# Kernel optimization log

Measured on AMD Instinct MI355X. Metric: run time of the kernel, lower is better.

## Reference

```python
import jax, jax.numpy as jnp
import numpy as np

EPS = 1e-5  # BatchNorm eps


def cbr(x, W, g, b, m, v):
    # 1x1 Conv (no bias) + inference BatchNorm + ReLU
    # x: [B,Cin,H,W], W: [Cout,Cin]
    y = jnp.einsum('oc,bchw->bohw', W, x)
    inv = g / jnp.sqrt(v + EPS)            # [Cout]
    y = y * inv[None, :, None, None] + (b - m * inv)[None, :, None, None]
    return jax.nn.relu(y)


def setup_inputs() -> dict:
    key = jax.random.key(0)
    ks = jax.random.split(key, 32)
    B, C, R, H, W = 4, 2048, 512, 64, 64
    d = {"feature": jax.random.normal(ks[0], (B, C, H, W), jnp.float32)}
    idx = 1
    for name, (cin, cout) in [("r", (C, R)), ("q", (R, R)), ("k", (R, R)), ("v", (R, R)), ("u", (R, C))]:
        d[name + "_W"] = jax.random.normal(ks[idx], (cout, cin), jnp.float32) * 0.02
        d[name + "_g"] = jax.random.uniform(ks[idx + 1], (cout,), jnp.float32)
        d[name + "_b"] = jax.random.normal(ks[idx + 2], (cout,), jnp.float32) * 0.1
        d[name + "_m"] = jax.random.normal(ks[idx + 3], (cout,), jnp.float32) * 0.1
        d[name + "_v"] = jax.random.uniform(ks[idx + 4], (cout,), jnp.float32)
        idx += 5
    return d


def reference(feature, r_W, r_g, r_b, r_m, r_v,
              q_W, q_g, q_b, q_m, q_v,
              k_W, k_g, k_b, k_m, k_v,
              v_W, v_g, v_b, v_m, v_v,
              u_W, u_g, u_b, u_m, u_v):
    B, C, H, W = feature.shape
    f = cbr(feature, r_W, r_g, r_b, r_m, r_v)          # [B,R,H,W]
    R = f.shape[1]
    N = H * W
    q = cbr(f, q_W, q_g, q_b, q_m, q_v).reshape(B, R, N)
    k = cbr(f, k_W, k_g, k_b, k_m, k_v).reshape(B, R, N)
    v = cbr(f, v_W, v_g, v_b, v_m, v_v).reshape(B, R, N)
    # similarity map over all spatial positions: [B,N,N]
    attn = jax.nn.softmax(jnp.einsum('bcn,bcm->bnm', q, k), axis=-1)
    upd = jnp.einsum('bnm,bcm->bnc', attn, v)          # [B,N,R]
    upd = upd.reshape(B, H, W, R).transpose(0, 3, 1, 2)  # [B,R,H,W]
    return cbr(f + upd, u_W, u_g, u_b, u_m, u_v)       # [B,C,H,W]
```

## Files before the change

kernel.cpp:

```cpp
#include <hip/hip_runtime.h>

#define EPSV 1e-5f

typedef unsigned short u16;
typedef __attribute__((ext_vector_type(8))) _Float16 half8;
typedef __attribute__((ext_vector_type(4))) float floatx4;

__device__ __forceinline__ float h2f(u16 h) {
    return (float)__builtin_bit_cast(_Float16, h);
}
__device__ __forceinline__ u16 f2h(float f) {
    _Float16 h = (_Float16)f;
    return __builtin_bit_cast(u16, h);
}

template <int MODE, typename OUTT>
__global__ __launch_bounds__(256)
void gemm_nt(const u16* __restrict__ A, const u16* __restrict__ B,
             OUTT* __restrict__ C_,
             const float* __restrict__ inv_, const float* __restrict__ beta_,
             const u16* __restrict__ addf,
             int K, int ldA, int ldB, int ldC,
             long strideA, long strideB, long strideC)
{
    __shared__ u16 As[4][128 * 32];
    __shared__ u16 Bs[4][128 * 32];

    const int tid = threadIdx.x;
    const int w = tid >> 6;
    const int l = tid & 63;

    int bx = blockIdx.x, by = blockIdx.y, bz = blockIdx.z;
    {
        const int gx = gridDim.x, gy = gridDim.y;
        const int nwg = gx * gy * (int)gridDim.z;
        if ((nwg & 7) == 0) {
            const int lin = bx + gx * (by + gy * bz);
            const int swz = (lin & 7) * (nwg >> 3) + (lin >> 3);
            bx = swz % gx;
            const int t = swz / gx;
            by = t % gy;
            bz = t / gy;
        }
    }
    const int j0 = bx * 128;
    const int i0 = by * 128;

    const u16* Ab = A + (long)bz * strideA;
    const u16* Bb = B + (long)bz * strideB;

    const int srow = w * 16 + (l >> 2);
    const int skel = (l & 3) * 8;

    const int i_base = (w >> 1) * 64;
    const int j_base = (w & 1) * 64;
    const int lm = l & 15;
    const int kq = l >> 4;

    floatx4 acc[4][4];
    #pragma unroll
    for (int a = 0; a < 4; ++a)
        #pragma unroll
        for (int b = 0; b < 4; ++b) acc[a][b] = (floatx4)(0.0f);

    auto stage = [&](int buf, int k0) {
        const u16* ga0 = Ab + (long)(i0 + srow) * ldA + k0 + skel;
        const u16* ga1 = Ab + (long)(i0 + 64 + srow) * ldA + k0 + skel;
        const u16* gb0 = Bb + (long)(j0 + srow) * ldB + k0 + skel;
        const u16* gb1 = Bb + (long)(j0 + 64 + srow) * ldB + k0 + skel;
        char* la0 = (char*)&As[buf][0] + w * 1024;
        char* la1 = (char*)&As[buf][0] + 4096 + w * 1024;
        char* lb0 = (char*)&Bs[buf][0] + w * 1024;
        char* lb1 = (char*)&Bs[buf][0] + 4096 + w * 1024;
        __builtin_amdgcn_global_load_lds(
            (const __attribute__((address_space(1))) unsigned int*)(const void*)ga0,
            (__attribute__((address_space(3))) unsigned int*)(void*)la0, 16, 0, 0);
        __builtin_amdgcn_global_load_lds(
            (const __attribute__((address_space(1))) unsigned int*)(const void*)ga1,
            (__attribute__((address_space(3))) unsigned int*)(void*)la1, 16, 0, 0);
        __builtin_amdgcn_global_load_lds(
            (const __attribute__((address_space(1))) unsigned int*)(const void*)gb0,
            (__attribute__((address_space(3))) unsigned int*)(void*)lb0, 16, 0, 0);
        __builtin_amdgcn_global_load_lds(
            (const __attribute__((address_space(1))) unsigned int*)(const void*)gb1,
            (__attribute__((address_space(3))) unsigned int*)(void*)lb1, 16, 0, 0);
    };

    const int nt = K >> 5;
    stage(0, 0);
    if (nt > 1) stage(1, 32);

    for (int t = 0; t < nt; ++t) {
        if (t + 2 < nt) {
            stage((t + 2) & 3, (t + 2) << 5);
            asm volatile("s_waitcnt vmcnt(8)" ::: "memory");
        } else if (t + 1 < nt) {
            asm volatile("s_waitcnt vmcnt(4)" ::: "memory");
        } else {
            asm volatile("s_waitcnt vmcnt(0)" ::: "memory");
        }
        __builtin_amdgcn_s_barrier();
        __builtin_amdgcn_sched_barrier(0);

        const u16* Ac = &As[t & 3][0];
        const u16* Bc = &Bs[t & 3][0];
        half8 af[4], bf[4];
        #pragma unroll
        for (int tt = 0; tt < 4; ++tt) {
            af[tt] = *(const half8*)&Ac[(i_base + tt * 16 + lm) * 32 + kq * 8];
            bf[tt] = *(const half8*)&Bc[(j_base + tt * 16 + lm) * 32 + kq * 8];
        }
        #pragma unroll
        for (int ti = 0; ti < 4; ++ti)
            #pragma unroll
            for (int tj = 0; tj < 4; ++tj)
                acc[ti][tj] = __builtin_amdgcn_mfma_f32_16x16x32_f16(
                    af[ti], bf[tj], acc[ti][tj], 0, 0, 0);
    }

    OUTT* Cb = C_ + (long)bz * strideC;
    const u16* addb = (MODE == 3) ? addf + (long)bz * strideC : nullptr;
    #pragma unroll
    for (int ti = 0; ti < 4; ++ti) {
        #pragma unroll
        for (int tj = 0; tj < 4; ++tj) {
            const int jj = j0 + j_base + tj * 16 + lm;
            float cinv = 0.f, cbeta = 0.f;
            if (MODE == 1) { cinv = inv_[jj]; cbeta = beta_[jj]; }
            #pragma unroll
            for (int r = 0; r < 4; ++r) {
                const int ii = i0 + i_base + ti * 16 + kq * 4 + r;
                float val = acc[ti][tj][r];
                if (MODE == 1) val = fmaxf(val * cinv + cbeta, 0.0f);
                if (MODE == 2) {
                    float iv = inv_[ii], bt = beta_[ii];
                    val = fmaxf(val * iv + bt, 0.0f);
                }
                if (MODE == 3) val += h2f(addb[(long)ii * ldC + jj]);
                if (sizeof(OUTT) == 4) {
                    ((float*)Cb)[(long)ii * ldC + jj] = val;
                } else {
                    ((u16*)Cb)[(long)ii * ldC + jj] = f2h(val);
                }
            }
        }
    }
}

__global__ __launch_bounds__(256)
void conv_weight(const float* __restrict__ W, const float* __restrict__ g,
                 const float* __restrict__ b, const float* __restrict__ m,
                 const float* __restrict__ v,
                 u16* __restrict__ Wb, float* __restrict__ inv_,
                 float* __restrict__ beta_, int cout, long n)
{
    for (long idx = (long)blockIdx.x * 256 + threadIdx.x; idx < n;
         idx += (long)gridDim.x * 256)
        Wb[idx] = f2h(W[idx]);
    int c = blockIdx.x * 256 + threadIdx.x;
    if (c < cout) {
        float iv = g[c] * rsqrtf(v[c] + EPSV);
        inv_[c] = iv;
        beta_[c] = b[c] - m[c] * iv;
    }
}

__global__ __launch_bounds__(256)
void transpose_conv(const float* __restrict__ in, u16* __restrict__ out,
                    int C, int N)
{
    __shared__ float t[32][33];
    const int n0 = blockIdx.x * 32, c0 = blockIdx.y * 32;
    const float* inb = in + (long)blockIdx.z * C * N;
    u16* outb = out + (long)blockIdx.z * C * N;
    const int tx = threadIdx.x & 31, ty = threadIdx.x >> 5;
    #pragma unroll
    for (int rr = 0; rr < 32; rr += 8)
        t[ty + rr][tx] = inb[(long)(c0 + ty + rr) * N + n0 + tx];
    __syncthreads();
    #pragma unroll
    for (int rr = 0; rr < 32; rr += 8)
        outb[(long)(n0 + ty + rr) * C + c0 + tx] = f2h(t[tx][ty + rr]);
}

__global__ __launch_bounds__(256)
void softmax_f16(const float* __restrict__ S, u16* __restrict__ P)
{
    __shared__ float buf[4096];
    __shared__ float red[256];
    const float* p = S + (long)blockIdx.y * 4096 * 4096 + (long)blockIdx.x * 4096;
    u16* o = P + (long)blockIdx.y * 4096 * 4096 + (long)blockIdx.x * 4096;
    const int tid = threadIdx.x;

    float lmax = -3.4e38f;
    for (int i = tid; i < 4096; i += 256) {
        float x = p[i];
        buf[i] = x;
        lmax = fmaxf(lmax, x);
    }
    red[tid] = lmax;
    __syncthreads();
    for (int s = 128; s > 0; s >>= 1) {
        if (tid < s) red[tid] = fmaxf(red[tid], red[tid + s]);
        __syncthreads();
    }
    const float mx = red[0];
    __syncthreads();

    float lsum = 0.0f;
    for (int i = tid; i < 4096; i += 256) {
        float e = __expf(buf[i] - mx);
        buf[i] = e;
        lsum += e;
    }
    red[tid] = lsum;
    __syncthreads();
    for (int s = 128; s > 0; s >>= 1) {
        if (tid < s) red[tid] += red[tid + s];
        __syncthreads();
    }
    const float invs = 1.0f / red[0];
    __syncthreads();

    for (int i = tid; i < 4096; i += 256) o[i] = f2h(buf[i] * invs);
}

extern "C" void kernel_launch(void* const* d_in, const int* in_sizes, int n_in,
                              void* d_out, int out_size, void* d_ws, size_t ws_size,
                              hipStream_t stream)
{
    (void)in_sizes; (void)n_in; (void)out_size; (void)ws_size;
    constexpr int B = 4, C = 2048, R = 512, N = 4096;
    constexpr long NR = (long)N * R;
    constexpr long NC = (long)N * C;
    constexpr long NN = (long)N * N;
    constexpr long NQK = (long)N * 1024;

    const float* feature = (const float*)d_in[0];
    const float* W_[5]  = {(const float*)d_in[1],  (const float*)d_in[6],
                           (const float*)d_in[11], (const float*)d_in[16],
                           (const float*)d_in[21]};
    const float* G_[5]  = {(const float*)d_in[2],  (const float*)d_in[7],
                           (const float*)d_in[12], (const float*)d_in[17],
                           (const float*)d_in[22]};
    const float* Bb_[5] = {(const float*)d_in[3],  (const float*)d_in[8],
                           (const float*)d_in[13], (const float*)d_in[18],
                           (const float*)d_in[23]};
    const float* M_[5]  = {(const float*)d_in[4],  (const float*)d_in[9],
                           (const float*)d_in[14], (const float*)d_in[19],
                           (const float*)d_in[24]};
    const float* V_[5]  = {(const float*)d_in[5],  (const float*)d_in[10],
                           (const float*)d_in[15], (const float*)d_in[20],
                           (const float*)d_in[25]};

    char* base = (char*)d_ws;
    size_t off = 0;
    float* S     = (float*)base;
    u16*   featT = (u16*)base;
    off += (size_t)B * NN * 4;
    u16* fT  = (u16*)(base + off);                     off += (size_t)B * NR * 2;
    u16* qkT = (u16*)(base + off);                     off += (size_t)B * NQK * 2;
    u16* vC  = (u16*)(base + off);                     off += (size_t)B * NR * 2;
    u16* gT  = (u16*)(base + off);                     off += (size_t)B * NR * 2;
    u16* Pc  = (u16*)(base + off);                     off += (size_t)B * NN * 2;
    u16* Wb_r  = (u16*)(base + off);  off += (size_t)R * C * 2;
    u16* WbQK  = (u16*)(base + off);  off += (size_t)1024 * R * 2;
    u16* Wb_v  = (u16*)(base + off);  off += (size_t)R * R * 2;
    u16* Wb_u  = (u16*)(base + off);  off += (size_t)C * R * 2;
    off = (off + 255) & ~(size_t)255;
    float* inv_r  = (float*)(base + off);  off += 8192;
    float* beta_r = (float*)(base + off);  off += 8192;
    float* invQK  = (float*)(base + off);  off += 8192;
    float* betaQK = (float*)(base + off);  off += 8192;
    float* inv_v  = (float*)(base + off);  off += 8192;
    float* beta_v = (float*)(base + off);  off += 8192;
    float* inv_u  = (float*)(base + off);  off += 8192;
    float* beta_u = (float*)(base + off);  off += 8192;

    float* out = (float*)d_out;
    const dim3 blk(256);

    conv_weight<<<512, blk, 0, stream>>>(W_[0], G_[0], Bb_[0], M_[0], V_[0],
                                         Wb_r, inv_r, beta_r, R, (long)R * C);
    conv_weight<<<512, blk, 0, stream>>>(W_[1], G_[1], Bb_[1], M_[1], V_[1],
                                         WbQK, invQK, betaQK, R, (long)R * R);
    conv_weight<<<512, blk, 0, stream>>>(W_[2], G_[2], Bb_[2], M_[2], V_[2],
                                         WbQK + (size_t)R * R, invQK + R, betaQK + R,
                                         R, (long)R * R);
    conv_weight<<<512, blk, 0, stream>>>(W_[3], G_[3], Bb_[3], M_[3], V_[3],
                                         Wb_v, inv_v, beta_v, R, (long)R * R);
    conv_weight<<<512, blk, 0, stream>>>(W_[4], G_[4], Bb_[4], M_[4], V_[4],
                                         Wb_u, inv_u, beta_u, C, (long)C * R);

    transpose_conv<<<dim3(N / 32, C / 32, B), blk, 0, stream>>>(feature, featT, C, N);

    gemm_nt<1, u16><<<dim3(R / 128, N / 128, B), blk, 0, stream>>>(
        featT, Wb_r, fT, inv_r, beta_r, nullptr,
        C, C, C, R, NC, 0, NR);

    gemm_nt<1, u16><<<dim3(1024 / 128, N / 128, B), blk, 0, stream>>>(
        fT, WbQK, qkT, invQK, betaQK, nullptr,
        R, R, R, 1024, NR, 0, NQK);

    gemm_nt<2, u16><<<dim3(N / 128, R / 128, B), blk, 0, stream>>>(
        Wb_v, fT, vC, inv_v, beta_v, nullptr,
        R, R, R, N, 0, NR, NR);

    gemm_nt<0, float><<<dim3(N / 128, N / 128, B), blk, 0, stream>>>(
        qkT, qkT + 512, S, nullptr, nullptr, nullptr,
        R, 1024, 1024, N, NQK, NQK, NN);

    softmax_f16<<<dim3(N, B), blk, 0, stream>>>(S, Pc);

    gemm_nt<3, u16><<<dim3(R / 128, N / 128, B), blk, 0, stream>>>(
        Pc, vC, gT, nullptr, nullptr, fT,
        N, N, N, R, NN, NR, NR);

    gemm_nt<2, float><<<dim3(N / 128, C / 128, B), blk, 0, stream>>>(
        Wb_u, gT, out, inv_u, beta_u, nullptr,
        R, R, R, N, 0, NR, NC);
}
```

Measured before the change: 801.5 us.

## Add double-buffer GEMM variant and split QK+softmax per batch

```diff
diff --git a/kernel.cpp b/kernel.cpp
--- a/kernel.cpp
+++ b/kernel.cpp
@@ -14,7 +14,7 @@
     return __builtin_bit_cast(u16, h);
 }
 
-template <int MODE, typename OUTT>
+template <int MODE, typename OUTT, int DEEP>
 __global__ __launch_bounds__(256)
 void gemm_nt(const u16* __restrict__ A, const u16* __restrict__ B,
              OUTT* __restrict__ C_,
@@ -23,8 +23,9 @@
              int K, int ldA, int ldB, int ldC,
              long strideA, long strideB, long strideC)
 {
-    __shared__ u16 As[4][128 * 32];
-    __shared__ u16 Bs[4][128 * 32];
+    constexpr int NBUF = DEEP ? 4 : 2;
+    __shared__ u16 As[NBUF][128 * 32];
+    __shared__ u16 Bs[NBUF][128 * 32];
 
     const int tid = threadIdx.x;
     const int w = tid >> 6;
@@ -87,35 +88,61 @@
     };
 
     const int nt = K >> 5;
-    stage(0, 0);
-    if (nt > 1) stage(1, 32);
-
-    for (int t = 0; t < nt; ++t) {
-        if (t + 2 < nt) {
-            stage((t + 2) & 3, (t + 2) << 5);
-            asm volatile("s_waitcnt vmcnt(8)" ::: "memory");
-        } else if (t + 1 < nt) {
-            asm volatile("s_waitcnt vmcnt(4)" ::: "memory");
-        } else {
-            asm volatile("s_waitcnt vmcnt(0)" ::: "memory");
+
+    if (DEEP) {
+        stage(0, 0);
+        if (nt > 1) stage(1, 32);
+        for (int t = 0; t < nt; ++t) {
+            if (t + 2 < nt) {
+                stage((t + 2) & 3, (t + 2) << 5);
+                asm volatile("s_waitcnt vmcnt(8)" ::: "memory");
+            } else if (t + 1 < nt) {
+                asm volatile("s_waitcnt vmcnt(4)" ::: "memory");
+            } else {
+                asm volatile("s_waitcnt vmcnt(0)" ::: "memory");
+            }
+            __builtin_amdgcn_s_barrier();
+            __builtin_amdgcn_sched_barrier(0);
+
+            const u16* Ac = &As[t & 3][0];
+            const u16* Bc = &Bs[t & 3][0];
+            half8 af[4], bf[4];
+            #pragma unroll
+            for (int tt = 0; tt < 4; ++tt) {
+                af[tt] = *(const half8*)&Ac[(i_base + tt * 16 + lm) * 32 + kq * 8];
+                bf[tt] = *(const half8*)&Bc[(j_base + tt * 16 + lm) * 32 + kq * 8];
+            }
+            #pragma unroll
+            for (int ti = 0; ti < 4; ++ti)
+                #pragma unroll
+                for (int tj = 0; tj < 4; ++tj)
+                    acc[ti][tj] = __builtin_amdgcn_mfma_f32_16x16x32_f16(
+                        af[ti], bf[tj], acc[ti][tj], 0, 0, 0);
         }
-        __builtin_amdgcn_s_barrier();
-        __builtin_amdgcn_sched_barrier(0);
-
-        const u16* Ac = &As[t & 3][0];
-        const u16* Bc = &Bs[t & 3][0];
-        half8 af[4], bf[4];
-        #pragma unroll
-        for (int tt = 0; tt < 4; ++tt) {
-            af[tt] = *(const half8*)&Ac[(i_base + tt * 16 + lm) * 32 + kq * 8];
-            bf[tt] = *(const half8*)&Bc[(j_base + tt * 16 + lm) * 32 + kq * 8];
+    } else {
+        stage(0, 0);
+        __syncthreads();
+        int cur = 0;
+        for (int t = 0; t < nt; ++t) {
+            if (t + 1 < nt) stage(cur ^ 1, (t + 1) << 5);
+
+            const u16* Ac = &As[cur][0];
+            const u16* Bc = &Bs[cur][0];
+            half8 af[4], bf[4];
+            #pragma unroll
+            for (int tt = 0; tt < 4; ++tt) {
+                af[tt] = *(const half8*)&Ac[(i_base + tt * 16 + lm) * 32 + kq * 8];
+                bf[tt] = *(const half8*)&Bc[(j_base + tt * 16 + lm) * 32 + kq * 8];
+            }
+            #pragma unroll
+            for (int ti = 0; ti < 4; ++ti)
+                #pragma unroll
+                for (int tj = 0; tj < 4; ++tj)
+                    acc[ti][tj] = __builtin_amdgcn_mfma_f32_16x16x32_f16(
+                        af[ti], bf[tj], acc[ti][tj], 0, 0, 0);
+            __syncthreads();
+            cur ^= 1;
         }
-        #pragma unroll
-        for (int ti = 0; ti < 4; ++ti)
-            #pragma unroll
-            for (int tj = 0; tj < 4; ++tj)
-                acc[ti][tj] = __builtin_amdgcn_mfma_f32_16x16x32_f16(
-                    af[ti], bf[tj], acc[ti][tj], 0, 0, 0);
     }
 
     OUTT* Cb = C_ + (long)bz * strideC;
@@ -188,8 +215,8 @@
 {
     __shared__ float buf[4096];
     __shared__ float red[256];
-    const float* p = S + (long)blockIdx.y * 4096 * 4096 + (long)blockIdx.x * 4096;
-    u16* o = P + (long)blockIdx.y * 4096 * 4096 + (long)blockIdx.x * 4096;
+    const float* p = S + (long)blockIdx.x * 4096;
+    u16* o = P + (long)blockIdx.x * 4096;
     const int tid = threadIdx.x;
 
     float lmax = -3.4e38f;
@@ -294,29 +321,32 @@
 
     transpose_conv<<<dim3(N / 32, C / 32, B), blk, 0, stream>>>(feature, featT, C, N);
 
-    gemm_nt<1, u16><<<dim3(R / 128, N / 128, B), blk, 0, stream>>>(
+    gemm_nt<1, u16, 1><<<dim3(R / 128, N / 128, B), blk, 0, stream>>>(
         featT, Wb_r, fT, inv_r, beta_r, nullptr,
         C, C, C, R, NC, 0, NR);
 
-    gemm_nt<1, u16><<<dim3(1024 / 128, N / 128, B), blk, 0, stream>>>(
+    gemm_nt<1, u16, 0><<<dim3(1024 / 128, N / 128, B), blk, 0, stream>>>(
         fT, WbQK, qkT, invQK, betaQK, nullptr,
         R, R, R, 1024, NR, 0, NQK);
 
-    gemm_nt<2, u16><<<dim3(N / 128, R / 128, B), blk, 0, stream>>>(
+    gemm_nt<2, u16, 1><<<dim3(N / 128, R / 128, B), blk, 0, stream>>>(
         Wb_v, fT, vC, inv_v, beta_v, nullptr,
         R, R, R, N, 0, NR, NR);
 
-    gemm_nt<0, float><<<dim3(N / 128, N / 128, B), blk, 0, stream>>>(
-        qkT, qkT + 512, S, nullptr, nullptr, nullptr,
-        R, 1024, 1024, N, NQK, NQK, NN);
-
-    softmax_f16<<<dim3(N, B), blk, 0, stream>>>(S, Pc);
-
-    gemm_nt<3, u16><<<dim3(R / 128, N / 128, B), blk, 0, stream>>>(
+    for (int b = 0; b < B; ++b) {
+        gemm_nt<0, float, 0><<<dim3(N / 128, N / 128, 1), blk, 0, stream>>>(
+            qkT + (long)b * NQK, qkT + (long)b * NQK + 512, S + (long)b * NN,
+            nullptr, nullptr, nullptr,
+            R, 1024, 1024, N, 0, 0, 0);
+        softmax_f16<<<dim3(N), blk, 0, stream>>>(S + (long)b * NN,
+                                                 Pc + (long)b * NN);
+    }
+
+    gemm_nt<3, u16, 1><<<dim3(R / 128, N / 128, B), blk, 0, stream>>>(
         Pc, vC, gT, nullptr, nullptr, fT,
         N, N, N, R, NN, NR, NR);
 
-    gemm_nt<2, float><<<dim3(N / 128, C / 128, B), blk, 0, stream>>>(
+    gemm_nt<2, float, 0><<<dim3(N / 128, C / 128, B), blk, 0, stream>>>(
         Wb_u, gT, out, inv_u, beta_u, nullptr,
         R, R, R, N, 0, NR, NC);
 }
```

Measured after the change: 779.7 us. -2.7%, faster.

## Enlarge GEMM tiles to 256x256 with 512 threads and split B staging

Applied to the files above, without the earlier changes.

```diff
diff --git a/kernel.cpp b/kernel.cpp
--- a/kernel.cpp
+++ b/kernel.cpp
@@ -14,17 +14,22 @@
     return __builtin_bit_cast(u16, h);
 }
 
+#define GLOAD_LDS(gsrc, ldst)                                                  \
+    __builtin_amdgcn_global_load_lds(                                          \
+        (const __attribute__((address_space(1))) unsigned int*)(const void*)(gsrc), \
+        (__attribute__((address_space(3))) unsigned int*)(void*)(ldst), 16, 0, 0)
+
 template <int MODE, typename OUTT>
-__global__ __launch_bounds__(256)
-void gemm_nt(const u16* __restrict__ A, const u16* __restrict__ B,
+__global__ __launch_bounds__(512, 1)
+void gemm256(const u16* __restrict__ A, const u16* __restrict__ B,
              OUTT* __restrict__ C_,
              const float* __restrict__ inv_, const float* __restrict__ beta_,
              const u16* __restrict__ addf,
              int K, int ldA, int ldB, int ldC,
              long strideA, long strideB, long strideC)
 {
-    __shared__ u16 As[4][128 * 32];
-    __shared__ u16 Bs[4][128 * 32];
+    __shared__ u16 As[4][256 * 32];
+    __shared__ u16 Bs[4][256 * 32];
 
     const int tid = threadIdx.x;
     const int w = tid >> 6;
@@ -38,13 +43,13 @@
             const int lin = bx + gx * (by + gy * bz);
             const int swz = (lin & 7) * (nwg >> 3) + (lin >> 3);
             bx = swz % gx;
-            const int t = swz / gx;
-            by = t % gy;
-            bz = t / gy;
-        }
-    }
-    const int j0 = bx * 128;
-    const int i0 = by * 128;
+            const int t2 = swz / gx;
+            by = t2 % gy;
+            bz = t2 / gy;
+        }
+    }
+    const int j0 = bx * 256;
+    const int i0 = by * 256;
 
     const u16* Ab = A + (long)bz * strideA;
     const u16* Bb = B + (long)bz * strideB;
@@ -52,48 +57,47 @@
     const int srow = w * 16 + (l >> 2);
     const int skel = (l & 3) * 8;
 
-    const int i_base = (w >> 1) * 64;
-    const int j_base = (w & 1) * 64;
+    const int wr = w >> 2;
+    const int wc = w & 3;
+    const int ibase = wr * 128;
+    const int jbase = wc * 64;
     const int lm = l & 15;
     const int kq = l >> 4;
 
-    floatx4 acc[4][4];
+    floatx4 acc[8][4];
     #pragma unroll
-    for (int a = 0; a < 4; ++a)
+    for (int a = 0; a < 8; ++a)
         #pragma unroll
         for (int b = 0; b < 4; ++b) acc[a][b] = (floatx4)(0.0f);
 
-    auto stage = [&](int buf, int k0) {
-        const u16* ga0 = Ab + (long)(i0 + srow) * ldA + k0 + skel;
-        const u16* ga1 = Ab + (long)(i0 + 64 + srow) * ldA + k0 + skel;
-        const u16* gb0 = Bb + (long)(j0 + srow) * ldB + k0 + skel;
-        const u16* gb1 = Bb + (long)(j0 + 64 + srow) * ldB + k0 + skel;
-        char* la0 = (char*)&As[buf][0] + w * 1024;
-        char* la1 = (char*)&As[buf][0] + 4096 + w * 1024;
-        char* lb0 = (char*)&Bs[buf][0] + w * 1024;
-        char* lb1 = (char*)&Bs[buf][0] + 4096 + w * 1024;
-        __builtin_amdgcn_global_load_lds(
-            (const __attribute__((address_space(1))) unsigned int*)(const void*)ga0,
-            (__attribute__((address_space(3))) unsigned int*)(void*)la0, 16, 0, 0);
-        __builtin_amdgcn_global_load_lds(
-            (const __attribute__((address_space(1))) unsigned int*)(const void*)ga1,
-            (__attribute__((address_space(3))) unsigned int*)(void*)la1, 16, 0, 0);
-        __builtin_amdgcn_global_load_lds(
-            (const __attribute__((address_space(1))) unsigned int*)(const void*)gb0,
-            (__attribute__((address_space(3))) unsigned int*)(void*)lb0, 16, 0, 0);
-        __builtin_amdgcn_global_load_lds(
-            (const __attribute__((address_space(1))) unsigned int*)(const void*)gb1,
-            (__attribute__((address_space(3))) unsigned int*)(void*)lb1, 16, 0, 0);
+    auto stageA = [&](int buf, int k0) {
+        #pragma unroll
+        for (int s = 0; s < 2; ++s) {
+            const u16* g = Ab + (long)(i0 + s * 128 + srow) * ldA + k0 + skel;
+            char* d = (char*)&As[buf][0] + (s * 128 + w * 16) * 64;
+            GLOAD_LDS(g, d);
+        }
     };
+    auto stageB = [&](int buf, int k0) {
+        #pragma unroll
+        for (int s = 0; s < 2; ++s) {
+            const u16* g = Bb + (long)(j0 + s * 128 + srow) * ldB + k0 + skel;
+            char* d = (char*)&Bs[buf][0] + (s * 128 + w * 16) * 64;
+            GLOAD_LDS(g, d);
+        }
+    };
 
     const int nt = K >> 5;
-    stage(0, 0);
-    if (nt > 1) stage(1, 32);
+    stageA(0, 0);  stageB(0, 0);
+    stageA(1, 32); stageB(1, 32);
 
     for (int t = 0; t < nt; ++t) {
+        const u16* Ac = &As[t & 3][0];
+        const u16* Bc = &Bs[t & 3][0];
+
         if (t + 2 < nt) {
-            stage((t + 2) & 3, (t + 2) << 5);
-            asm volatile("s_waitcnt vmcnt(8)" ::: "memory");
+            stageA((t + 2) & 3, (t + 2) << 5);
+            asm volatile("s_waitcnt vmcnt(6)" ::: "memory");
         } else if (t + 1 < nt) {
             asm volatile("s_waitcnt vmcnt(4)" ::: "memory");
         } else {
@@ -102,34 +106,53 @@
         __builtin_amdgcn_s_barrier();
         __builtin_amdgcn_sched_barrier(0);
 
-        const u16* Ac = &As[t & 3][0];
-        const u16* Bc = &Bs[t & 3][0];
-        half8 af[4], bf[4];
-        #pragma unroll
-        for (int tt = 0; tt < 4; ++tt) {
-            af[tt] = *(const half8*)&Ac[(i_base + tt * 16 + lm) * 32 + kq * 8];
-            bf[tt] = *(const half8*)&Bc[(j_base + tt * 16 + lm) * 32 + kq * 8];
-        }
-        #pragma unroll
-        for (int ti = 0; ti < 4; ++ti)
+        half8 af[8], bf[4];
+        #pragma unroll
+        for (int m = 0; m < 8; ++m)
+            af[m] = *(const half8*)&Ac[(ibase + m * 16 + lm) * 32 + kq * 8];
+        #pragma unroll
+        for (int n = 0; n < 2; ++n)
+            bf[n] = *(const half8*)&Bc[(jbase + n * 16 + lm) * 32 + kq * 8];
+        asm volatile("s_waitcnt lgkmcnt(0)" ::: "memory");
+        __builtin_amdgcn_sched_barrier(0);
+        __builtin_amdgcn_s_setprio(1);
+        #pragma unroll
+        for (int m = 0; m < 8; ++m)
             #pragma unroll
-            for (int tj = 0; tj < 4; ++tj)
-                acc[ti][tj] = __builtin_amdgcn_mfma_f32_16x16x32_f16(
-                    af[ti], bf[tj], acc[ti][tj], 0, 0, 0);
+            for (int n = 0; n < 2; ++n)
+                acc[m][n] = __builtin_amdgcn_mfma_f32_16x16x32_f16(
+                    af[m], bf[n], acc[m][n], 0, 0, 0);
+        __builtin_amdgcn_s_setprio(0);
+
+        if (t + 2 < nt) stageB((t + 2) & 3, (t + 2) << 5);
+        #pragma unroll
+        for (int n = 2; n < 4; ++n)
+            bf[n] = *(const half8*)&Bc[(jbase + n * 16 + lm) * 32 + kq * 8];
+        asm volatile("s_waitcnt lgkmcnt(0)" ::: "memory");
+        __builtin_amdgcn_sched_barrier(0);
+        __builtin_amdgcn_s_setprio(1);
+        #pragma unroll
+        for (int m = 0; m < 8; ++m)
+            #pragma unroll
+            for (int n = 2; n < 4; ++n)
+                acc[m][n] = __builtin_amdgcn_mfma_f32_16x16x32_f16(
+                    af[m], bf[n], acc[m][n], 0, 0, 0);
+        __builtin_amdgcn_s_setprio(0);
+        __builtin_amdgcn_s_barrier();
     }
 
     OUTT* Cb = C_ + (long)bz * strideC;
     const u16* addb = (MODE == 3) ? addf + (long)bz * strideC : nullptr;
     #pragma unroll
-    for (int ti = 0; ti < 4; ++ti) {
+    for (int ti = 0; ti < 8; ++ti) {
         #pragma unroll
         for (int tj = 0; tj < 4; ++tj) {
-            const int jj = j0 + j_base + tj * 16 + lm;
+            const int jj = j0 + jbase + tj * 16 + lm;
             float cinv = 0.f, cbeta = 0.f;
             if (MODE == 1) { cinv = inv_[jj]; cbeta = beta_[jj]; }
             #pragma unroll
             for (int r = 0; r < 4; ++r) {
-                const int ii = i0 + i_base + ti * 16 + kq * 4 + r;
+                const int ii = i0 + ibase + ti * 16 + kq * 4 + r;
                 float val = acc[ti][tj][r];
                 if (MODE == 1) val = fmaxf(val * cinv + cbeta, 0.0f);
                 if (MODE == 2) {
@@ -188,8 +211,8 @@
 {
     __shared__ float buf[4096];
     __shared__ float red[256];
-    const float* p = S + (long)blockIdx.y * 4096 * 4096 + (long)blockIdx.x * 4096;
-    u16* o = P + (long)blockIdx.y * 4096 * 4096 + (long)blockIdx.x * 4096;
+    const float* p = S + (long)blockIdx.x * 4096;
+    u16* o = P + (long)blockIdx.x * 4096;
     const int tid = threadIdx.x;
 
     float lmax = -3.4e38f;
@@ -279,6 +302,7 @@
 
     float* out = (float*)d_out;
     const dim3 blk(256);
+    const dim3 blk512(512);
 
     conv_weight<<<512, blk, 0, stream>>>(W_[0], G_[0], Bb_[0], M_[0], V_[0],
                                          Wb_r, inv_r, beta_r, R, (long)R * C);
@@ -294,29 +318,32 @@
 
     transpose_conv<<<dim3(N / 32, C / 32, B), blk, 0, stream>>>(feature, featT, C, N);
 
-    gemm_nt<1, u16><<<dim3(R / 128, N / 128, B), blk, 0, stream>>>(
+    gemm256<1, u16><<<dim3(R / 256, (B * N) / 256, 1), blk512, 0, stream>>>(
         featT, Wb_r, fT, inv_r, beta_r, nullptr,
-        C, C, C, R, NC, 0, NR);
-
-    gemm_nt<1, u16><<<dim3(1024 / 128, N / 128, B), blk, 0, stream>>>(
+        C, C, C, R, 0, 0, 0);
+
+    gemm256<1, u16><<<dim3(1024 / 256, (B * N) / 256, 1), blk512, 0, stream>>>(
         fT, WbQK, qkT, invQK, betaQK, nullptr,
-        R, R, R, 1024, NR, 0, NQK);
-
-    gemm_nt<2, u16><<<dim3(N / 128, R / 128, B), blk, 0, stream>>>(
+        R, R, R, 1024, 0, 0, 0);
+
+    gemm256<2, u16><<<dim3(N / 256, R / 256, B), blk512, 0, stream>>>(
         Wb_v, fT, vC, inv_v, beta_v, nullptr,
         R, R, R, N, 0, NR, NR);
 
-    gemm_nt<0, float><<<dim3(N / 128, N / 128, B), blk, 0, stream>>>(
-        qkT, qkT + 512, S, nullptr, nullptr, nullptr,
-        R, 1024, 1024, N, NQK, NQK, NN);
-
-    softmax_f16<<<dim3(N, B), blk, 0, stream>>>(S, Pc);
-
-    gemm_nt<3, u16><<<dim3(R / 128, N / 128, B), blk, 0, stream>>>(
+    for (int b = 0; b < B; ++b) {
+        gemm256<0, float><<<dim3(N / 256, N / 256, 1), blk512, 0, stream>>>(
+            qkT + (long)b * NQK, qkT + (long)b * NQK + 512, S + (long)b * NN,
+            nullptr, nullptr, nullptr,
+            R, 1024, 1024, N, 0, 0, 0);
+        softmax_f16<<<dim3(N), blk, 0, stream>>>(S + (long)b * NN,
+                                                 Pc + (long)b * NN);
+    }
+
+    gemm256<3, u16><<<dim3(R / 256, N / 256, B), blk512, 0, stream>>>(
         Pc, vC, gT, nullptr, nullptr, fT,
         N, N, N, R, NN, NR, NR);
 
-    gemm_nt<2, float><<<dim3(N / 128, C / 128, B), blk, 0, stream>>>(
+    gemm256<2, float><<<dim3(N / 256, C / 256, B), blk512, 0, stream>>>(
         Wb_u, gT, out, inv_u, beta_u, nullptr,
         R, R, R, N, 0, NR, NC);
 }
```

Result: slower. 908.0 us (+13.3%).
